# Kernel optimization log

Measured on AMD Instinct MI355X. Metric: run time of the kernel, lower is better.

## Reference

```python
import jax, jax.numpy as jnp
import numpy as np

N = 100000
E = 1600000
IN_C, HID_C, OUT_C = 512, 128, 64
BN_EPS = 1e-5


def _add_self_loops(edge_index, n):
    loops = jnp.arange(n, dtype=edge_index.dtype)
    row = jnp.concatenate([edge_index[0], loops])
    col = jnp.concatenate([edge_index[1], loops])
    return row, col


def gcn_conv(x, W, b, row, col, n):
    # PyG GCNConv: linear first, then symmetric-normalized aggregation
    h = x @ W                                        # [N, out]
    ones = jnp.ones(row.shape[0], dtype=x.dtype)
    deg = jax.ops.segment_sum(ones, col, num_segments=n)   # in-degree incl. self-loop
    dinv = jax.lax.rsqrt(deg)                        # deg >= 1 due to self-loops
    norm = dinv[row] * dinv[col]                     # [E2]
    msg = h[row] * norm[:, None]                     # gather + scale
    out = jax.ops.segment_sum(msg, col, num_segments=n)    # scatter-add
    return out + b


def batchnorm_train(x, gamma, beta):
    mu = jnp.mean(x, axis=0)
    var = jnp.mean((x - mu) ** 2, axis=0)            # biased var, as torch BN
    return (x - mu) * jax.lax.rsqrt(var + BN_EPS) * gamma + beta


def setup_inputs() -> dict:
    key = jax.random.key(0)
    ks = jax.random.split(key, 8)
    x = jax.random.normal(ks[0], (N, IN_C), dtype=jnp.float32)
    edge_index = jax.random.randint(ks[1], (2, E), 0, N, dtype=jnp.int64)
    W1 = jax.random.normal(ks[2], (IN_C, HID_C), dtype=jnp.float32) / np.sqrt(IN_C)
    b1 = jnp.zeros((HID_C,), dtype=jnp.float32)
    gamma = jnp.ones((HID_C,), dtype=jnp.float32)
    beta = jnp.zeros((HID_C,), dtype=jnp.float32)
    W2 = jax.random.normal(ks[3], (HID_C, OUT_C), dtype=jnp.float32) / np.sqrt(HID_C)
    b2 = jnp.zeros((OUT_C,), dtype=jnp.float32)
    return {"x": x, "edge_index": edge_index, "W1": W1, "b1": b1,
            "gamma": gamma, "beta": beta, "W2": W2, "b2": b2}


def reference(x, edge_index, W1, b1, gamma, beta, W2, b2):
    row, col = _add_self_loops(edge_index, N)
    h = gcn_conv(x, W1, b1, row, col, N)
    h = batchnorm_train(h, gamma, beta)
    h = jax.nn.relu(h)
    # dropout: identity (deterministic reference)
    out = gcn_conv(h, W2, b2, row, col, N)
    return out
```

## Files before the change

kernel.cpp:

```cpp
#include <hip/hip_runtime.h>

#define NN 100000
#define NE 1600000
#define INC 512
#define HID 128
#define OUTC 64
#define BN_EPS 1e-5f

#define GS_B 1024
#define NSCB 98

#define NBLK 256
#define CHUNK (NE / NBLK)
#define BSH 8
#define NBUK ((NN + 255) >> 8)

typedef __attribute__((ext_vector_type(8))) short short8v;
typedef __attribute__((ext_vector_type(4))) float f32x4;

__device__ __forceinline__ unsigned short f2bf(float f) {
    unsigned u = __float_as_uint(f);
    u += 0x7FFFu + ((u >> 16) & 1u);
    return (unsigned short)(u >> 16);
}

__device__ __forceinline__ unsigned cvtpk(float lo, float hi) {
    unsigned r;
    asm("v_cvt_pk_bf16_f32 %0, %1, %2" : "=v"(r) : "v"(lo), "v"(hi));
    return r;
}

__device__ __forceinline__ float bflo(unsigned u) { return __uint_as_float(u << 16); }
__device__ __forceinline__ float bfhi(unsigned u) { return __uint_as_float(u & 0xFFFF0000u); }

__device__ __forceinline__ void scan_bsum(const int* __restrict__ bsum2, int* spref) {
    int tid = threadIdx.x;
    if (tid < NSCB) spref[tid] = bsum2[tid];
    __syncthreads();
    if (tid == 0) {
        int run = 0;
        #pragma unroll 1
        for (int i = 0; i < NSCB; ++i) { int t = spref[i]; spref[i] = run; run += t; }
    }
    __syncthreads();
}


__global__ __launch_bounds__(256) void k_pre(const int* __restrict__ col, int* __restrict__ bhist,
                                             const float* __restrict__ W1, unsigned short* __restrict__ W1T,
                                             float* bnsum, float* bnsumsq) {
    __shared__ int lc[NBUK];
    int tid = threadIdx.x, blk = blockIdx.x;
    int i = blk * 256 + tid;
    W1T[(size_t)(i & 127) * INC + (i >> 7)] = f2bf(W1[i]);
    if (blk == 0 && tid < HID) { bnsum[tid] = 0.f; bnsumsq[tid] = 0.f; }
    for (int q = tid; q < NBUK; q += 256) lc[q] = 0;
    __syncthreads();
    int s = blk * CHUNK, e = s + CHUNK;
    for (int j = s + tid; j < e; j += 256)
        atomicAdd(&lc[col[j] >> BSH], 1);
    __syncthreads();
    for (int q = tid; q < NBUK; q += 256)
        bhist[q * NBLK + blk] = lc[q];
}

__global__ void k_gscanA(const int* __restrict__ src, int* __restrict__ dst,
                         int* __restrict__ bsum, int n) {
    __shared__ int s[GS_B];
    int tid = threadIdx.x;
    int i = blockIdx.x * GS_B + tid;
    int v = (i < n) ? src[i] : 0;
    s[tid] = v;
    __syncthreads();
    for (int off = 1; off < GS_B; off <<= 1) {
        int t = (tid >= off) ? s[tid - off] : 0;
        __syncthreads();
        s[tid] += t;
        __syncthreads();
    }
    if (i < n) dst[i] = s[tid] - v;
    if (tid == GS_B - 1) bsum[blockIdx.x] = s[tid];
}

__global__ __launch_bounds__(256) void k_bpart(const int* __restrict__ row, const int* __restrict__ col,
                                               const int* __restrict__ sb, const int* __restrict__ bsum2,
                                               unsigned* __restrict__ ebuk) {
    __shared__ int lcur[NBUK];
    __shared__ int spref[NSCB];
    int tid = threadIdx.x, blk = blockIdx.x;
    scan_bsum(bsum2, spref);
    for (int i = tid; i < NBUK; i += 256) {
        int idx = i * NBLK + blk;
        lcur[i] = sb[idx] + spref[idx >> 10];
    }
    __syncthreads();
    int s = blk * CHUNK, e = s + CHUNK;
    for (int j = s + tid; j < e; j += 256) {
        int r = row[j], c = col[j];
        int p = atomicAdd(&lcur[c >> BSH], 1);
        ebuk[p] = (unsigned)r | ((unsigned)(c & 255) << 24);
    }
}

__global__ __launch_bounds__(256) void k_nprep(const unsigned* __restrict__ ebuk,
                                               const int* __restrict__ sb, const int* __restrict__ bsum2,
                                               int* __restrict__ deg, int* __restrict__ rowptr) {
    __shared__ int lc[256];
    __shared__ int sc[256];
    __shared__ int spref[NSCB];
    int b = blockIdx.x, tid = threadIdx.x;
    scan_bsum(bsum2, spref);
    lc[tid] = 0;
    __syncthreads();
    int i0 = b * NBLK;
    int s = sb[i0] + spref[i0 >> 10];
    int e2 = (b + 1 < NBUK) ? (sb[i0 + NBLK] + spref[(i0 + NBLK) >> 10]) : NE;
    for (int j = s + tid; j < e2; j += 256)
        atomicAdd(&lc[ebuk[j] >> 24], 1);
    __syncthreads();
    int v = lc[tid];
    sc[tid] = v;
    __syncthreads();
    for (int off = 1; off < 256; off <<= 1) {
        int t = (tid >= off) ? sc[tid - off] : 0;
        __syncthreads();
        sc[tid] += t;
        __syncthreads();
    }
    int node = (b << BSH) + tid;
    if (node < NN) {
        deg[node] = v;
        rowptr[node] = s + sc[tid] - v;
    }
    if (b == NBUK - 1 && tid == 0) rowptr[NN] = NE;
}

__global__ __launch_bounds__(256) void k_bfill(const unsigned* __restrict__ ebuk,
                                               const int* __restrict__ sb, const int* __restrict__ bsum2,
                                               const int* __restrict__ rowptr, const int* __restrict__ deg,
                                               unsigned* __restrict__ csr) {
    __shared__ int lcur[256];
    __shared__ int spref[NSCB];
    int b = blockIdx.x, tid = threadIdx.x;
    scan_bsum(bsum2, spref);
    int node0 = b << BSH;
    int node = node0 + tid;
    lcur[tid] = (node < NN) ? rowptr[node] : 0;
    __syncthreads();
    int i0 = b * NBLK;
    int s = sb[i0] + spref[i0 >> 10];
    int e2 = (b + 1 < NBUK) ? (sb[i0 + NBLK] + spref[(i0 + NBLK) >> 10]) : NE;
    for (int j = s + tid; j < e2; j += 256) {
        unsigned rc = ebuk[j];
        int li = rc >> 24;
        int r = rc & 0xFFFFFF;
        int p = atomicAdd(&lcur[li], 1);
        csr[p] = (unsigned)r | ((unsigned)deg[r] << 17);
    }
}


#define G1BK 64
#define APAD 72

__global__ __launch_bounds__(256) void k_gemm1m(const float* __restrict__ x,
                                                const unsigned short* __restrict__ W1T,
                                                unsigned short* __restrict__ h1b) {
    __shared__ unsigned short As[64][APAD];
    __shared__ unsigned short Bs[128][APAD];
    int tid = threadIdx.x;
    int m0 = blockIdx.x * 64;
    int w = tid >> 6;
    int lane = tid & 63;

    f32x4 acc[4][2];
    #pragma unroll
    for (int mr = 0; mr < 4; ++mr)
        #pragma unroll
        for (int cb = 0; cb < 2; ++cb) acc[mr][cb] = (f32x4){0.f, 0.f, 0.f, 0.f};

    int ar = tid >> 2;
    int ak = (tid & 3) * 16;
    int arow = m0 + ar; if (arow >= NN) arow = NN - 1;
    const float* xr = x + (size_t)arow * INC;
    int br = tid >> 1;
    int bk = (tid & 1) * 32;
    const unsigned short* wr = W1T + (size_t)br * INC;

    int frow = lane & 15;
    int fk = (lane >> 4) * 8;

    float4 pv[4];
    short8v pb[4];
    #pragma unroll
    for (int q = 0; q < 4; ++q) pv[q] = *(const float4*)(xr + ak + q * 4);
    #pragma unroll
    for (int q = 0; q < 4; ++q) pb[q] = *(const short8v*)(wr + bk + q * 8);

    for (int k0 = 0; k0 < INC; k0 += G1BK) {
        #pragma unroll
        for (int q = 0; q < 4; ++q)
            *(uint2*)&As[ar][ak + q * 4] = make_uint2(cvtpk(pv[q].x, pv[q].y), cvtpk(pv[q].z, pv[q].w));
        #pragma unroll
        for (int q = 0; q < 4; ++q)
            *(short8v*)&Bs[br][bk + q * 8] = pb[q];
        __syncthreads();
        if (k0 + G1BK < INC) {
            #pragma unroll
            for (int q = 0; q < 4; ++q) pv[q] = *(const float4*)(xr + k0 + G1BK + ak + q * 4);
            #pragma unroll
            for (int q = 0; q < 4; ++q) pb[q] = *(const short8v*)(wr + k0 + G1BK + bk + q * 8);
        }
        #pragma unroll
        for (int kk = 0; kk < G1BK; kk += 32) {
            short8v a[4], b[2];
            #pragma unroll
            for (int mr = 0; mr < 4; ++mr)
                a[mr] = *(const short8v*)&As[16 * mr + frow][kk + fk];
            #pragma unroll
            for (int cb = 0; cb < 2; ++cb)
                b[cb] = *(const short8v*)&Bs[32 * w + 16 * cb + frow][kk + fk];
            #pragma unroll
            for (int mr = 0; mr < 4; ++mr)
                #pragma unroll
                for (int cb = 0; cb < 2; ++cb)
                    acc[mr][cb] = __builtin_amdgcn_mfma_f32_16x16x32_bf16(b[cb], a[mr], acc[mr][cb], 0, 0, 0);
        }
        __syncthreads();
    }
    int ncol = lane & 15;
    int r4 = (lane >> 4) * 4;
    #pragma unroll
    for (int mr = 0; mr < 4; ++mr) {
        int node = m0 + 16 * mr + ncol;
        if (node < NN) {
            #pragma unroll
            for (int cb = 0; cb < 2; ++cb) {
                int ch = 32 * w + 16 * cb + r4;
                *(uint2*)&h1b[(size_t)node * HID + ch] =
                    make_uint2(cvtpk(acc[mr][cb][0], acc[mr][cb][1]),
                               cvtpk(acc[mr][cb][2], acc[mr][cb][3]));
            }
        }
    }
}


__global__ __launch_bounds__(256) void k_agg1(const unsigned short* __restrict__ h1b,
                                              const int* __restrict__ deg,
                                              const int* __restrict__ rowptr, const unsigned* __restrict__ csr,
                                              const float* __restrict__ b1, unsigned* __restrict__ aggb) {
    int node = blockIdx.x * 4 + (threadIdx.x >> 6);
    int lane = threadIdx.x & 63;
    const unsigned* hp = (const unsigned*)h1b;
    size_t base = (size_t)node * 64 + lane;
    float dnf = (float)(deg[node] + 1);
    float di = rsqrtf(dnf);
    float wself = di * di;
    unsigned hv = hp[base];
    float sx = wself * bflo(hv);
    float sy = wself * bfhi(hv);
    int s = rowptr[node], e = rowptr[node + 1];
    int j = s;
    for (; j + 8 <= e; j += 8) {
        unsigned c0 = csr[j],     c1 = csr[j + 1], c2 = csr[j + 2], c3 = csr[j + 3];
        unsigned c4 = csr[j + 4], c5 = csr[j + 5], c6 = csr[j + 6], c7 = csr[j + 7];
        unsigned v0 = hp[(size_t)(c0 & 0x1FFFF) * 64 + lane];
        unsigned v1 = hp[(size_t)(c1 & 0x1FFFF) * 64 + lane];
        unsigned v2 = hp[(size_t)(c2 & 0x1FFFF) * 64 + lane];
        unsigned v3 = hp[(size_t)(c3 & 0x1FFFF) * 64 + lane];
        unsigned v4 = hp[(size_t)(c4 & 0x1FFFF) * 64 + lane];
        unsigned v5 = hp[(size_t)(c5 & 0x1FFFF) * 64 + lane];
        unsigned v6 = hp[(size_t)(c6 & 0x1FFFF) * 64 + lane];
        unsigned v7 = hp[(size_t)(c7 & 0x1FFFF) * 64 + lane];
        float w0 = rsqrtf(dnf * (float)((c0 >> 17) + 1));
        float w1 = rsqrtf(dnf * (float)((c1 >> 17) + 1));
        float w2 = rsqrtf(dnf * (float)((c2 >> 17) + 1));
        float w3 = rsqrtf(dnf * (float)((c3 >> 17) + 1));
        float w4 = rsqrtf(dnf * (float)((c4 >> 17) + 1));
        float w5 = rsqrtf(dnf * (float)((c5 >> 17) + 1));
        float w6 = rsqrtf(dnf * (float)((c6 >> 17) + 1));
        float w7 = rsqrtf(dnf * (float)((c7 >> 17) + 1));
        sx = fmaf(w0, bflo(v0), sx); sy = fmaf(w0, bfhi(v0), sy);
        sx = fmaf(w1, bflo(v1), sx); sy = fmaf(w1, bfhi(v1), sy);
        sx = fmaf(w2, bflo(v2), sx); sy = fmaf(w2, bfhi(v2), sy);
        sx = fmaf(w3, bflo(v3), sx); sy = fmaf(w3, bfhi(v3), sy);
        sx = fmaf(w4, bflo(v4), sx); sy = fmaf(w4, bfhi(v4), sy);
        sx = fmaf(w5, bflo(v5), sx); sy = fmaf(w5, bfhi(v5), sy);
        sx = fmaf(w6, bflo(v6), sx); sy = fmaf(w6, bfhi(v6), sy);
        sx = fmaf(w7, bflo(v7), sx); sy = fmaf(w7, bfhi(v7), sy);
    }
    for (; j + 4 <= e; j += 4) {
        unsigned c0 = csr[j], c1 = csr[j + 1], c2 = csr[j + 2], c3 = csr[j + 3];
        unsigned v0 = hp[(size_t)(c0 & 0x1FFFF) * 64 + lane];
        unsigned v1 = hp[(size_t)(c1 & 0x1FFFF) * 64 + lane];
        unsigned v2 = hp[(size_t)(c2 & 0x1FFFF) * 64 + lane];
        unsigned v3 = hp[(size_t)(c3 & 0x1FFFF) * 64 + lane];
        float w0 = rsqrtf(dnf * (float)((c0 >> 17) + 1));
        float w1 = rsqrtf(dnf * (float)((c1 >> 17) + 1));
        float w2 = rsqrtf(dnf * (float)((c2 >> 17) + 1));
        float w3 = rsqrtf(dnf * (float)((c3 >> 17) + 1));
        sx = fmaf(w0, bflo(v0), sx); sy = fmaf(w0, bfhi(v0), sy);
        sx = fmaf(w1, bflo(v1), sx); sy = fmaf(w1, bfhi(v1), sy);
        sx = fmaf(w2, bflo(v2), sx); sy = fmaf(w2, bfhi(v2), sy);
        sx = fmaf(w3, bflo(v3), sx); sy = fmaf(w3, bfhi(v3), sy);
    }
    for (; j < e; ++j) {
        unsigned c = csr[j];
        unsigned v = hp[(size_t)(c & 0x1FFFF) * 64 + lane];
        float ww = rsqrtf(dnf * (float)((c >> 17) + 1));
        sx = fmaf(ww, bflo(v), sx); sy = fmaf(ww, bfhi(v), sy);
    }
    float2 bb = ((const float2*)b1)[lane];
    aggb[base] = cvtpk(sx + bb.x, sy + bb.y);
}


__global__ __launch_bounds__(256) void k_bnstats(const unsigned* __restrict__ aggb,
                                                 float* __restrict__ bnsum, float* __restrict__ bnsumsq) {
    __shared__ float4 ss[256], sq[256];
    int g = threadIdx.x & 31;
    int h = threadIdx.x >> 5;
    float4 fs = make_float4(0.f, 0.f, 0.f, 0.f);
    float4 fq = make_float4(0.f, 0.f, 0.f, 0.f);
    int rows_per_block = (NN + gridDim.x - 1) / gridDim.x;
    int r0 = blockIdx.x * rows_per_block;
    int r1 = r0 + rows_per_block; if (r1 > NN) r1 = NN;
    for (int r = r0 + h; r < r1; r += 8) {
        uint2 u = *(const uint2*)(aggb + (size_t)r * 64 + 2 * g);
        float a0 = bflo(u.x), a1 = bfhi(u.x), a2 = bflo(u.y), a3 = bfhi(u.y);
        fs.x += a0; fs.y += a1; fs.z += a2; fs.w += a3;
        fq.x += a0 * a0; fq.y += a1 * a1; fq.z += a2 * a2; fq.w += a3 * a3;
    }
    ss[threadIdx.x] = fs; sq[threadIdx.x] = fq;
    __syncthreads();
    if (threadIdx.x < 32) {
        float4 as = ss[threadIdx.x], aq = sq[threadIdx.x];
        #pragma unroll
        for (int k = 1; k < 8; ++k) {
            float4 bs = ss[k * 32 + threadIdx.x], bq = sq[k * 32 + threadIdx.x];
            as.x += bs.x; as.y += bs.y; as.z += bs.z; as.w += bs.w;
            aq.x += bq.x; aq.y += bq.y; aq.z += bq.z; aq.w += bq.w;
        }
        atomicAdd(&bnsum[4 * g + 0], as.x); atomicAdd(&bnsum[4 * g + 1], as.y);
        atomicAdd(&bnsum[4 * g + 2], as.z); atomicAdd(&bnsum[4 * g + 3], as.w);
        atomicAdd(&bnsumsq[4 * g + 0], aq.x); atomicAdd(&bnsumsq[4 * g + 1], aq.y);
        atomicAdd(&bnsumsq[4 * g + 2], aq.z); atomicAdd(&bnsumsq[4 * g + 3], aq.w);
    }
}


__global__ __launch_bounds__(256) void k_gemm2(const unsigned* __restrict__ aggb, const float* __restrict__ W2,
                                               const float* __restrict__ bnsum, const float* __restrict__ bnsumsq,
                                               const float* __restrict__ gamma, const float* __restrict__ beta,
                                               unsigned short* __restrict__ h2b) {
    __shared__ float As2[32][66];
    __shared__ float Bs2[32][OUTC];
    __shared__ float bnsc[HID], bnsh[HID];
    int tid = threadIdx.x;
    if (tid < HID) {
        float mu = bnsum[tid] / (float)NN;
        float var = bnsumsq[tid] / (float)NN - mu * mu;
        float sc = gamma[tid] * rsqrtf(var + BN_EPS);
        bnsc[tid] = sc;
        bnsh[tid] = beta[tid] - mu * sc;
    }
    __syncthreads();
    int m0 = blockIdx.x * 64;
    int tx = tid & 15, ty = tid >> 4;
    float acc[4][4];
    #pragma unroll
    for (int r = 0; r < 4; ++r)
        #pragma unroll
        for (int c = 0; c < 4; ++c) acc[r][c] = 0.f;

    int am = tid >> 3;
    int ak = (tid & 7) * 4;
    int bk = tid >> 4;
    int bc = (tid & 15) * 4;

    for (int k0 = 0; k0 < HID; k0 += 32) {
        #pragma unroll
        for (int h = 0; h < 2; ++h) {
            int m = am + h * 32;
            int rowi = m0 + m; if (rowi >= NN) rowi = NN - 1;
            uint2 u = *(const uint2*)(aggb + (size_t)rowi * 64 + ((k0 + ak) >> 1));
            float4 sc = *(const float4*)&bnsc[k0 + ak];
            float4 sh = *(const float4*)&bnsh[k0 + ak];
            As2[ak + 0][m] = fmaxf(fmaf(bflo(u.x), sc.x, sh.x), 0.f);
            As2[ak + 1][m] = fmaxf(fmaf(bfhi(u.x), sc.y, sh.y), 0.f);
            As2[ak + 2][m] = fmaxf(fmaf(bflo(u.y), sc.z, sh.z), 0.f);
            As2[ak + 3][m] = fmaxf(fmaf(bfhi(u.y), sc.w, sh.w), 0.f);
        }
        #pragma unroll
        for (int h = 0; h < 2; ++h) {
            int k = bk + h * 16;
            *(float4*)&Bs2[k][bc] = *(const float4*)(W2 + (size_t)(k0 + k) * OUTC + bc);
        }
        __syncthreads();
        #pragma unroll
        for (int k = 0; k < 32; ++k) {
            float a[4];
            #pragma unroll
            for (int r = 0; r < 4; ++r) a[r] = As2[k][ty * 4 + r];
            float4 b = *(const float4*)&Bs2[k][tx * 4];
            #pragma unroll
            for (int r = 0; r < 4; ++r) {
                acc[r][0] = fmaf(a[r], b.x, acc[r][0]);
                acc[r][1] = fmaf(a[r], b.y, acc[r][1]);
                acc[r][2] = fmaf(a[r], b.z, acc[r][2]);
                acc[r][3] = fmaf(a[r], b.w, acc[r][3]);
            }
        }
        __syncthreads();
    }
    #pragma unroll
    for (int r = 0; r < 4; ++r) {
        int m = m0 + ty * 4 + r;
        if (m < NN) {
            *(uint2*)(h2b + (size_t)m * OUTC + tx * 4) =
                make_uint2(cvtpk(acc[r][0], acc[r][1]), cvtpk(acc[r][2], acc[r][3]));
        }
    }
}


__global__ __launch_bounds__(256) void k_agg2(const unsigned short* __restrict__ h2b,
                                              const int* __restrict__ deg,
                                              const int* __restrict__ rowptr, const unsigned* __restrict__ csr,
                                              const float* __restrict__ b2, float* __restrict__ out) {
    int node = blockIdx.x * 4 + (threadIdx.x >> 6);
    int lane = threadIdx.x & 63;
    int l32 = lane & 31;
    const unsigned* hp = (const unsigned*)h2b;
    float dnf = (float)(deg[node] + 1);
    float di = rsqrtf(dnf);
    float wself = di * di;
    float sx = 0.f, sy = 0.f;
    if (lane < 32) {
        unsigned u = hp[(size_t)node * 32 + l32];
        sx = wself * bflo(u);
        sy = wself * bfhi(u);
    }
    int s = rowptr[node], e = rowptr[node + 1];
    int j = s + (lane >> 5);
    for (; j + 6 < e; j += 8) {
        unsigned c0 = csr[j], c1 = csr[j + 2], c2 = csr[j + 4], c3 = csr[j + 6];
        unsigned v0 = hp[(size_t)(c0 & 0x1FFFF) * 32 + l32];
        unsigned v1 = hp[(size_t)(c1 & 0x1FFFF) * 32 + l32];
        unsigned v2 = hp[(size_t)(c2 & 0x1FFFF) * 32 + l32];
        unsigned v3 = hp[(size_t)(c3 & 0x1FFFF) * 32 + l32];
        float w0 = rsqrtf(dnf * (float)((c0 >> 17) + 1));
        float w1 = rsqrtf(dnf * (float)((c1 >> 17) + 1));
        float w2 = rsqrtf(dnf * (float)((c2 >> 17) + 1));
        float w3 = rsqrtf(dnf * (float)((c3 >> 17) + 1));
        sx = fmaf(w0, bflo(v0), sx); sy = fmaf(w0, bfhi(v0), sy);
        sx = fmaf(w1, bflo(v1), sx); sy = fmaf(w1, bfhi(v1), sy);
        sx = fmaf(w2, bflo(v2), sx); sy = fmaf(w2, bfhi(v2), sy);
        sx = fmaf(w3, bflo(v3), sx); sy = fmaf(w3, bfhi(v3), sy);
    }
    for (; j + 2 < e; j += 4) {
        unsigned c0 = csr[j], c1 = csr[j + 2];
        unsigned v0 = hp[(size_t)(c0 & 0x1FFFF) * 32 + l32];
        unsigned v1 = hp[(size_t)(c1 & 0x1FFFF) * 32 + l32];
        float w0 = rsqrtf(dnf * (float)((c0 >> 17) + 1));
        float w1 = rsqrtf(dnf * (float)((c1 >> 17) + 1));
        sx = fmaf(w0, bflo(v0), sx); sy = fmaf(w0, bfhi(v0), sy);
        sx = fmaf(w1, bflo(v1), sx); sy = fmaf(w1, bfhi(v1), sy);
    }
    if (j < e) {
        unsigned c = csr[j];
        unsigned v = hp[(size_t)(c & 0x1FFFF) * 32 + l32];
        float ww = rsqrtf(dnf * (float)((c >> 17) + 1));
        sx = fmaf(ww, bflo(v), sx); sy = fmaf(ww, bfhi(v), sy);
    }
    sx += __shfl_xor(sx, 32);
    sy += __shfl_xor(sy, 32);
    if (lane < 32) {
        float2 bb = ((const float2*)b2)[l32];
        ((float2*)out)[(size_t)node * 32 + l32] = make_float2(sx + bb.x, sy + bb.y);
    }
}


extern "C" void kernel_launch(void* const* d_in, const int* in_sizes, int n_in,
                              void* d_out, int out_size, void* d_ws, size_t ws_size,
                              hipStream_t stream) {
    const float* x     = (const float*)d_in[0];
    const int*   ei    = (const int*)d_in[1];
    const float* W1    = (const float*)d_in[2];
    const float* b1    = (const float*)d_in[3];
    const float* gamma = (const float*)d_in[4];
    const float* beta  = (const float*)d_in[5];
    const float* W2    = (const float*)d_in[6];
    const float* b2    = (const float*)d_in[7];
    const int* row = ei;
    const int* col = ei + NE;
    float* out = (float*)d_out;

    char* wp = (char*)d_ws;
    auto alloc = [&](size_t bytes) -> void* {
        void* p = (void*)wp;
        wp += (bytes + 255) & ~(size_t)255;
        return p;
    };
    unsigned short* h1b = (unsigned short*)alloc((size_t)NN * HID * 2);
    unsigned* aggb = (unsigned*)alloc((size_t)NN * HID * 2);
    unsigned short* h2b = (unsigned short*)alloc((size_t)NN * OUTC * 2);
    int*   deg     = (int*)alloc((size_t)NN * 4);
    float* bnsum   = (float*)alloc(HID * 4);
    float* bnsumsq = (float*)alloc(HID * 4);
    int*   rowptr  = (int*)alloc((size_t)(NN + 1) * 4);
    int*   bhist   = (int*)alloc((size_t)NBUK * NBLK * 4);
    int*   bsum2   = (int*)alloc(NSCB * 4);
    unsigned* ebuk = (unsigned*)alloc((size_t)NE * 4);
    unsigned* csr  = (unsigned*)alloc((size_t)NE * 4);
    unsigned short* W1T = (unsigned short*)alloc((size_t)HID * INC * 2);

    hipLaunchKernelGGL(k_pre,    dim3(NBLK), dim3(256), 0, stream, col, bhist, W1, W1T, bnsum, bnsumsq);
    hipLaunchKernelGGL(k_gscanA, dim3(NSCB), dim3(GS_B), 0, stream, bhist, bhist, bsum2, NBUK * NBLK);
    hipLaunchKernelGGL(k_bpart,  dim3(NBLK), dim3(256), 0, stream, row, col, bhist, bsum2, ebuk);
    hipLaunchKernelGGL(k_nprep,  dim3(NBUK), dim3(256), 0, stream, ebuk, bhist, bsum2, deg, rowptr);
    hipLaunchKernelGGL(k_bfill,  dim3(NBUK), dim3(256), 0, stream, ebuk, bhist, bsum2, rowptr, deg, csr);
    hipLaunchKernelGGL(k_gemm1m, dim3((NN + 63) / 64), dim3(256), 0, stream, x, W1T, h1b);
    hipLaunchKernelGGL(k_agg1,   dim3(NN / 4), dim3(256), 0, stream, h1b, deg, rowptr, csr, b1, aggb);
    hipLaunchKernelGGL(k_bnstats, dim3(256), dim3(256), 0, stream, aggb, bnsum, bnsumsq);
    hipLaunchKernelGGL(k_gemm2,  dim3((NN + 63) / 64), dim3(256), 0, stream, aggb, W2, bnsum, bnsumsq, gamma, beta, h2b);
    hipLaunchKernelGGL(k_agg2,   dim3(NN / 4), dim3(256), 0, stream, h2b, deg, rowptr, csr, b2, out);
}
```

Baseline: 313.0 us.

## Co-schedule GEMM1 tiles with CSR build kernels via block-index dispatch

Splits the first dense GEMM's 1563 row tiles across the three CSR construction kernels (bucket partition, node prep, fill). Extra blocks in each launch run GEMM tiles while the others do the graph work, so the latency-bound scatter stages overlap with compute and the separate GEMM launch goes away. Shared memory is now one union buffer sized for the GEMM, which may lower occupancy for the CSR blocks. The aggregation kernels also compute degree from rowptr differences instead of loading the deg array.

```diff
diff --git a/kernel.cpp b/kernel.cpp
--- a/kernel.cpp
+++ b/kernel.cpp
@@ -14,6 +14,14 @@
 #define CHUNK (NE / NBLK)
 #define BSH 8
 #define NBUK ((NN + 255) >> 8)
+
+#define G1_TOTAL 1563
+#define G1A 704
+#define G1B 288
+#define G1C 571
+
+#define APAD 72
+#define SMEM_BYTES (64 * APAD * 2 + 128 * APAD * 2)
 
 typedef __attribute__((ext_vector_type(8))) short short8v;
 typedef __attribute__((ext_vector_type(4))) float f32x4;
@@ -82,12 +90,13 @@
     if (tid == GS_B - 1) bsum[blockIdx.x] = s[tid];
 }
 
-__global__ __launch_bounds__(256) void k_bpart(const int* __restrict__ row, const int* __restrict__ col,
-                                               const int* __restrict__ sb, const int* __restrict__ bsum2,
-                                               unsigned* __restrict__ ebuk) {
-    __shared__ int lcur[NBUK];
-    __shared__ int spref[NSCB];
-    int tid = threadIdx.x, blk = blockIdx.x;
+
+__device__ void dev_bpart(char* smem, const int* __restrict__ row, const int* __restrict__ col,
+                          const int* __restrict__ sb, const int* __restrict__ bsum2,
+                          unsigned* __restrict__ ebuk, int blk) {
+    int* lcur = (int*)smem;
+    int* spref = (int*)(smem + ((NBUK * 4 + 15) & ~15));
+    int tid = threadIdx.x;
     scan_bsum(bsum2, spref);
     for (int i = tid; i < NBUK; i += 256) {
         int idx = i * NBLK + blk;
@@ -102,13 +111,13 @@
     }
 }
 
-__global__ __launch_bounds__(256) void k_nprep(const unsigned* __restrict__ ebuk,
-                                               const int* __restrict__ sb, const int* __restrict__ bsum2,
-                                               int* __restrict__ deg, int* __restrict__ rowptr) {
-    __shared__ int lc[256];
-    __shared__ int sc[256];
-    __shared__ int spref[NSCB];
-    int b = blockIdx.x, tid = threadIdx.x;
+__device__ void dev_nprep(char* smem, const unsigned* __restrict__ ebuk,
+                          const int* __restrict__ sb, const int* __restrict__ bsum2,
+                          int* __restrict__ deg, int* __restrict__ rowptr, int b) {
+    int* lc = (int*)smem;
+    int* sc = (int*)(smem + 1024);
+    int* spref = (int*)(smem + 2048);
+    int tid = threadIdx.x;
     scan_bsum(bsum2, spref);
     lc[tid] = 0;
     __syncthreads();
@@ -135,13 +144,13 @@
     if (b == NBUK - 1 && tid == 0) rowptr[NN] = NE;
 }
 
-__global__ __launch_bounds__(256) void k_bfill(const unsigned* __restrict__ ebuk,
-                                               const int* __restrict__ sb, const int* __restrict__ bsum2,
-                                               const int* __restrict__ rowptr, const int* __restrict__ deg,
-                                               unsigned* __restrict__ csr) {
-    __shared__ int lcur[256];
-    __shared__ int spref[NSCB];
-    int b = blockIdx.x, tid = threadIdx.x;
+__device__ void dev_bfill(char* smem, const unsigned* __restrict__ ebuk,
+                          const int* __restrict__ sb, const int* __restrict__ bsum2,
+                          const int* __restrict__ rowptr, const int* __restrict__ deg,
+                          unsigned* __restrict__ csr, int b) {
+    int* lcur = (int*)smem;
+    int* spref = (int*)(smem + 1024);
+    int tid = threadIdx.x;
     scan_bsum(bsum2, spref);
     int node0 = b << BSH;
     int node = node0 + tid;
@@ -159,17 +168,15 @@
     }
 }
 
-
 #define G1BK 64
-#define APAD 72
-
-__global__ __launch_bounds__(256) void k_gemm1m(const float* __restrict__ x,
-                                                const unsigned short* __restrict__ W1T,
-                                                unsigned short* __restrict__ h1b) {
-    __shared__ unsigned short As[64][APAD];
-    __shared__ unsigned short Bs[128][APAD];
-    int tid = threadIdx.x;
-    int m0 = blockIdx.x * 64;
+
+__device__ void dev_gemm1(char* smem, const float* __restrict__ x,
+                          const unsigned short* __restrict__ W1T,
+                          unsigned short* __restrict__ h1b, int mblk) {
+    unsigned short (*As)[APAD] = (unsigned short (*)[APAD])smem;
+    unsigned short (*Bs)[APAD] = (unsigned short (*)[APAD])(smem + 64 * APAD * 2);
+    int tid = threadIdx.x;
+    int m0 = mblk * 64;
     int w = tid >> 6;
     int lane = tid & 63;
 
@@ -246,21 +253,55 @@
 }
 
 
+__global__ __launch_bounds__(256) void k_fuse1(const int* __restrict__ row, const int* __restrict__ col,
+                                               const int* __restrict__ sb, const int* __restrict__ bsum2,
+                                               unsigned* __restrict__ ebuk,
+                                               const float* __restrict__ x,
+                                               const unsigned short* __restrict__ W1T,
+                                               unsigned short* __restrict__ h1b) {
+    __shared__ __align__(16) char smem[SMEM_BYTES];
+    if (blockIdx.x < NBLK) dev_bpart(smem, row, col, sb, bsum2, ebuk, blockIdx.x);
+    else                   dev_gemm1(smem, x, W1T, h1b, blockIdx.x - NBLK);
+}
+
+__global__ __launch_bounds__(256) void k_fuse2(const unsigned* __restrict__ ebuk,
+                                               const int* __restrict__ sb, const int* __restrict__ bsum2,
+                                               int* __restrict__ deg, int* __restrict__ rowptr,
+                                               const float* __restrict__ x,
+                                               const unsigned short* __restrict__ W1T,
+                                               unsigned short* __restrict__ h1b) {
+    __shared__ __align__(16) char smem[SMEM_BYTES];
+    if (blockIdx.x < NBUK) dev_nprep(smem, ebuk, sb, bsum2, deg, rowptr, blockIdx.x);
+    else                   dev_gemm1(smem, x, W1T, h1b, blockIdx.x - NBUK + G1A);
+}
+
+__global__ __launch_bounds__(256) void k_fuse3(const unsigned* __restrict__ ebuk,
+                                               const int* __restrict__ sb, const int* __restrict__ bsum2,
+                                               const int* __restrict__ rowptr, const int* __restrict__ deg,
+                                               unsigned* __restrict__ csr,
+                                               const float* __restrict__ x,
+                                               const unsigned short* __restrict__ W1T,
+                                               unsigned short* __restrict__ h1b) {
+    __shared__ __align__(16) char smem[SMEM_BYTES];
+    if (blockIdx.x < NBUK) dev_bfill(smem, ebuk, sb, bsum2, rowptr, deg, csr, blockIdx.x);
+    else                   dev_gemm1(smem, x, W1T, h1b, blockIdx.x - NBUK + G1A + G1B);
+}
+
+
 __global__ __launch_bounds__(256) void k_agg1(const unsigned short* __restrict__ h1b,
-                                              const int* __restrict__ deg,
                                               const int* __restrict__ rowptr, const unsigned* __restrict__ csr,
                                               const float* __restrict__ b1, unsigned* __restrict__ aggb) {
     int node = blockIdx.x * 4 + (threadIdx.x >> 6);
     int lane = threadIdx.x & 63;
     const unsigned* hp = (const unsigned*)h1b;
     size_t base = (size_t)node * 64 + lane;
-    float dnf = (float)(deg[node] + 1);
+    int s = rowptr[node], e = rowptr[node + 1];
+    float dnf = (float)(e - s + 1);
     float di = rsqrtf(dnf);
     float wself = di * di;
     unsigned hv = hp[base];
     float sx = wself * bflo(hv);
     float sy = wself * bfhi(hv);
-    int s = rowptr[node], e = rowptr[node + 1];
     int j = s;
     for (; j + 8 <= e; j += 8) {
         unsigned c0 = csr[j],     c1 = csr[j + 1], c2 = csr[j + 2], c3 = csr[j + 3];
@@ -426,14 +467,14 @@
 
 
 __global__ __launch_bounds__(256) void k_agg2(const unsigned short* __restrict__ h2b,
-                                              const int* __restrict__ deg,
                                               const int* __restrict__ rowptr, const unsigned* __restrict__ csr,
                                               const float* __restrict__ b2, float* __restrict__ out) {
     int node = blockIdx.x * 4 + (threadIdx.x >> 6);
     int lane = threadIdx.x & 63;
     int l32 = lane & 31;
     const unsigned* hp = (const unsigned*)h2b;
-    float dnf = (float)(deg[node] + 1);
+    int s = rowptr[node], e = rowptr[node + 1];
+    float dnf = (float)(e - s + 1);
     float di = rsqrtf(dnf);
     float wself = di * di;
     float sx = 0.f, sy = 0.f;
@@ -442,7 +483,6 @@
         sx = wself * bflo(u);
         sy = wself * bfhi(u);
     }
-    int s = rowptr[node], e = rowptr[node + 1];
     int j = s + (lane >> 5);
     for (; j + 6 < e; j += 8) {
         unsigned c0 = csr[j], c1 = csr[j + 2], c2 = csr[j + 4], c3 = csr[j + 6];
@@ -519,12 +559,11 @@
 
     hipLaunchKernelGGL(k_pre,    dim3(NBLK), dim3(256), 0, stream, col, bhist, W1, W1T, bnsum, bnsumsq);
     hipLaunchKernelGGL(k_gscanA, dim3(NSCB), dim3(GS_B), 0, stream, bhist, bhist, bsum2, NBUK * NBLK);
-    hipLaunchKernelGGL(k_bpart,  dim3(NBLK), dim3(256), 0, stream, row, col, bhist, bsum2, ebuk);
-    hipLaunchKernelGGL(k_nprep,  dim3(NBUK), dim3(256), 0, stream, ebuk, bhist, bsum2, deg, rowptr);
-    hipLaunchKernelGGL(k_bfill,  dim3(NBUK), dim3(256), 0, stream, ebuk, bhist, bsum2, rowptr, deg, csr);
-    hipLaunchKernelGGL(k_gemm1m, dim3((NN + 63) / 64), dim3(256), 0, stream, x, W1T, h1b);
-    hipLaunchKernelGGL(k_agg1,   dim3(NN / 4), dim3(256), 0, stream, h1b, deg, rowptr, csr, b1, aggb);
+    hipLaunchKernelGGL(k_fuse1,  dim3(NBLK + G1A), dim3(256), 0, stream, row, col, bhist, bsum2, ebuk, x, W1T, h1b);
+    hipLaunchKernelGGL(k_fuse2,  dim3(NBUK + G1B), dim3(256), 0, stream, ebuk, bhist, bsum2, deg, rowptr, x, W1T, h1b);
+    hipLaunchKernelGGL(k_fuse3,  dim3(NBUK + G1C), dim3(256), 0, stream, ebuk, bhist, bsum2, rowptr, deg, csr, x, W1T, h1b);
+    hipLaunchKernelGGL(k_agg1,   dim3(NN / 4), dim3(256), 0, stream, h1b, rowptr, csr, b1, aggb);
     hipLaunchKernelGGL(k_bnstats, dim3(256), dim3(256), 0, stream, aggb, bnsum, bnsumsq);
     hipLaunchKernelGGL(k_gemm2,  dim3((NN + 63) / 64), dim3(256), 0, stream, aggb, W2, bnsum, bnsumsq, gamma, beta, h2b);
-    hipLaunchKernelGGL(k_agg2,   dim3(NN / 4), dim3(256), 0, stream, h2b, deg, rowptr, csr, b2, out);
-}
+    hipLaunchKernelGGL(k_agg2,   dim3(NN / 4), dim3(256), 0, stream, h2b, rowptr, csr, b2, out);
+}
```

New measurement: 311.3 us. About the same (-0.5%).
